# Kernel optimization log

Measured on AMD Instinct MI355X. Metric: run time of the kernel, lower is better.

## Reference

```python
import jax, jax.numpy as jnp
import numpy as np

N = 100000
IN_C, HID, OUT_D, NUM_CLASSES = 256, 64, 64, 6
E = 1600000


def setup_inputs() -> dict:
    key = jax.random.key(0)
    ks = jax.random.split(key, 12)
    glorot = lambda k, fi, fo: jax.random.normal(k, (fi, fo), jnp.float32) * np.sqrt(2.0 / (fi + fo))
    return {
        "x": jax.random.normal(ks[0], (N, IN_C), jnp.float32),
        "edge_index": jax.random.randint(ks[1], (2, E), 0, N, jnp.int64),
        "W1": glorot(ks[2], IN_C, HID), "b1": jnp.zeros((HID,), jnp.float32),
        "W2": glorot(ks[3], HID, HID), "b2": jnp.zeros((HID,), jnp.float32),
        "Wp": glorot(ks[4], HID, OUT_D), "bp": jnp.zeros((OUT_D,), jnp.float32),
        "Wc": glorot(ks[5], OUT_D, NUM_CLASSES), "bc": jnp.zeros((NUM_CLASSES,), jnp.float32),
    }


def _gcn_norm(edge_index, n):
    # add self-loops, symmetric normalization D^{-1/2}(A+I)D^{-1/2} (PyG gcn_norm)
    loop = jnp.arange(n, dtype=edge_index.dtype)
    src = jnp.concatenate([edge_index[0], loop])
    dst = jnp.concatenate([edge_index[1], loop])
    deg = jax.ops.segment_sum(jnp.ones_like(dst, jnp.float32), dst, num_segments=n)
    dinv = jnp.where(deg > 0, jax.lax.rsqrt(deg), 0.0)
    norm = dinv[src] * dinv[dst]  # [E+N]
    return src, dst, norm


def _gcn_conv(x, W, b, src, dst, norm, n):
    h = x @ W  # dense GEMM first (PyG order)
    msg = h[src] * norm[:, None]  # gather + scale over edges
    out = jax.ops.segment_sum(msg, dst, num_segments=n)  # scatter-add aggregate
    return out + b


def reference(x, edge_index, W1, b1, W2, b2, Wp, bp, Wc, bc):
    n = x.shape[0]
    src, dst, norm = _gcn_norm(edge_index, n)
    h = jax.nn.relu(_gcn_conv(x, W1, b1, src, dst, norm, n))
    # dropout is inactive in eval mode (training=False)
    h = jax.nn.relu(_gcn_conv(h, W2, b2, src, dst, norm, n))
    z = jax.nn.relu(h @ Wp + bp)
    logits = z @ Wc + bc
    return (logits, z)
```

## Files before the change

kernel.cpp:

```cpp
#include <hip/hip_runtime.h>

#define N_NODES 100000
#define IN_CH   256
#define HID_D   64
#define NCLS    6
#define NE      1600000
#define WB      48
#define OVF_CAP 4096
#define NPART   8
#define PSZ     (N_NODES / NPART)

typedef unsigned short u16;
typedef unsigned int   u32;
typedef __attribute__((ext_vector_type(8))) short bf16x8;
typedef __attribute__((ext_vector_type(4))) float f32x4;
typedef __attribute__((ext_vector_type(2))) int   i32x2;

#define OFF_CNT   0u
#define OFF_OVFC  400000u
#define OFF_OVF   400128u
#define OFF_COL   433152u
#define OFF_WT    19633152u
#define OFF_G     19684480u
#define OFF_H     32484480u
#define WT_W1 0
#define WT_W2 16384
#define WT_WP 20480
#define WT_WC 24576
#define WT_TOT 25600
#define Z_OFF 600000u

__device__ __forceinline__ u16 f2bf(float f) {
    u32 u = __float_as_uint(f);
    return (u16)((u + 0x7fffu + ((u >> 16) & 1u)) >> 16);
}
__device__ __forceinline__ float bf2f(u16 h) {
    return __uint_as_float(((u32)h) << 16);
}

__global__ __launch_bounds__(256) void k_wprep(const float* __restrict__ W1,
                                               const float* __restrict__ W2,
                                               const float* __restrict__ Wp,
                                               const float* __restrict__ Wc,
                                               u16* __restrict__ wt) {
    int m = blockIdx.x * 256 + threadIdx.x;
    if (m >= WT_TOT) return;
    float v;
    if (m >= WT_WC) {
        int i = m - WT_WC;
        int j = i & 7, l = (i >> 3) & 63, kk = i >> 9;
        int k = kk * 32 + (l >> 4) * 8 + j;
        int c = l & 15;
        v = (c < NCLS) ? Wc[k * NCLS + c] : 0.f;
    } else {
        const float* src; int i;
        if      (m < WT_W2) { src = W1; i = m - WT_W1; }
        else if (m < WT_WP) { src = W2; i = m - WT_W2; }
        else                { src = Wp; i = m - WT_WP; }
        int j = i & 7, l = (i >> 3) & 63, t = (i >> 9) & 3, kk = i >> 11;
        int k = kk * 32 + (l >> 4) * 8 + j;
        int c = t * 16 + (l & 15);
        v = src[k * 64 + c];
    }
    wt[m] = f2bf(v);
}

__global__ __launch_bounds__(256) void k_fill(const int* __restrict__ ei,
                                              int* __restrict__ cnt,
                                              int* __restrict__ col,
                                              int* __restrict__ ovfc,
                                              int* __restrict__ ovf) {
    const int part = blockIdx.x & (NPART - 1);
    const int lo = part * PSZ;
    const int hi = lo + PSZ;
    const int e0 = (blockIdx.x >> 3) * 512 + threadIdx.x * 2;
    i32x2 s2 = __builtin_nontemporal_load((const i32x2*)(ei + e0));
    i32x2 d2 = __builtin_nontemporal_load((const i32x2*)(ei + NE + e0));
#pragma unroll
    for (int j = 0; j < 2; ++j) {
        int s = s2[j];
        int d = d2[j];
        if (d < lo || d >= hi) continue;
        if ((u32)s >= (u32)N_NODES) continue;
        int p = atomicAdd(&cnt[d], 1);
        if (p < WB) {
            col[(size_t)d * WB + p] = s;
        } else {
            int k = atomicAdd(ovfc, 1);
            if (k < OVF_CAP) { ovf[2 * k] = s; ovf[2 * k + 1] = d; }
        }
    }
}

template <int KDIM, bool ABF16>
__global__ __launch_bounds__(256) void k_gemm(const void* __restrict__ A,
                                              const u16* __restrict__ wt,
                                              const int* __restrict__ cnt,
                                              u16* __restrict__ G) {
    constexpr int KK = KDIM / 32;
    __shared__ __align__(16) u16 sB[KK * 2048];

    for (int idx = threadIdx.x * 8; idx < KK * 2048; idx += 2048)
        *(bf16x8*)&sB[idx] = *(const bf16x8*)&wt[idx];
    __syncthreads();

    const int lane = threadIdx.x & 63;
    const int wv   = threadIdx.x >> 6;
    const int row0 = blockIdx.x * 64 + wv * 16;
    const int g4   = lane >> 4;
    const int r16  = lane & 15;

    int arow = row0 + r16;
    int arow_c = arow < N_NODES ? arow : 0;

    f32x4 acc[4] = {{0,0,0,0},{0,0,0,0},{0,0,0,0},{0,0,0,0}};

#pragma unroll
    for (int kk = 0; kk < KK; ++kk) {
        bf16x8 a;
        if (ABF16) {
            a = *(const bf16x8*)((const u16*)A + (size_t)arow_c * KDIM + kk * 32 + g4 * 8);
        } else {
            const float* ap = (const float*)A + (size_t)arow_c * KDIM + kk * 32 + g4 * 8;
            float4 f0 = *(const float4*)ap;
            float4 f1 = *(const float4*)(ap + 4);
            a[0] = (short)f2bf(f0.x); a[1] = (short)f2bf(f0.y);
            a[2] = (short)f2bf(f0.z); a[3] = (short)f2bf(f0.w);
            a[4] = (short)f2bf(f1.x); a[5] = (short)f2bf(f1.y);
            a[6] = (short)f2bf(f1.z); a[7] = (short)f2bf(f1.w);
        }
#pragma unroll
        for (int t = 0; t < 4; ++t) {
            bf16x8 b = *(const bf16x8*)&sB[((kk * 4 + t) * 64 + lane) * 8];
            acc[t] = __builtin_amdgcn_mfma_f32_16x16x32_bf16(a, b, acc[t], 0, 0, 0);
        }
    }

#pragma unroll
    for (int r = 0; r < 4; ++r) {
        int row = row0 + g4 * 4 + r;
        if (row < N_NODES) {
            float dinv = rsqrtf((float)(cnt[row] + 1));
#pragma unroll
            for (int t = 0; t < 4; ++t)
                G[(size_t)row * 64 + t * 16 + r16] = f2bf(acc[t][r] * dinv);
        }
    }
}

__global__ __launch_bounds__(256) void k_agg(const u16* __restrict__ G,
                                             const int* __restrict__ col,
                                             const int* __restrict__ cnt,
                                             const int* __restrict__ ovfc,
                                             const int* __restrict__ ovf,
                                             const float* __restrict__ bias,
                                             u16* __restrict__ Hout) {
    int node = blockIdx.x * 4 + (threadIdx.x >> 6);
    int lane = threadIdx.x & 63;

    int deg = cnt[node];
    int m = min(deg, WB);
    int mycol = (lane < WB) ? col[(size_t)node * WB + lane] : 0;

    float acc = bf2f(G[(size_t)node * 64 + lane]);

    int e = 0;
    for (; e + 4 <= m; e += 4) {
        int c0 = __shfl(mycol, e + 0), c1 = __shfl(mycol, e + 1);
        int c2 = __shfl(mycol, e + 2), c3 = __shfl(mycol, e + 3);
        float v0 = bf2f(G[(size_t)c0 * 64 + lane]);
        float v1 = bf2f(G[(size_t)c1 * 64 + lane]);
        float v2 = bf2f(G[(size_t)c2 * 64 + lane]);
        float v3 = bf2f(G[(size_t)c3 * 64 + lane]);
        acc += v0; acc += v1; acc += v2; acc += v3;
    }
    for (; e < m; ++e) {
        int c = __shfl(mycol, e);
        acc += bf2f(G[(size_t)c * 64 + lane]);
    }

    int no = *ovfc;
    if (no > 0) {
        no = min(no, OVF_CAP);
        for (int j = 0; j < no; ++j)
            if (ovf[2 * j + 1] == node)
                acc += bf2f(G[(size_t)ovf[2 * j] * 64 + lane]);
    }

    float dinv = rsqrtf((float)(deg + 1));
    float v = fmaxf(acc * dinv + bias[lane], 0.f);
    Hout[(size_t)node * 64 + lane] = f2bf(v);
}

__global__ __launch_bounds__(256) void k_mlp(const u16* __restrict__ H,
                                             const u16* __restrict__ wt,
                                             const float* __restrict__ bp,
                                             const float* __restrict__ bc,
                                             float* __restrict__ out) {
    __shared__ __align__(16) u16 sP[2 * 2048];
    __shared__ __align__(16) u16 sC[1024];
    __shared__ __align__(16) u16 zt[4][16][72];

    for (int idx = threadIdx.x * 8; idx < 4096; idx += 2048)
        *(bf16x8*)&sP[idx] = *(const bf16x8*)&wt[WT_WP + idx];
    {
        int idx = threadIdx.x * 8;
        if (idx < 1024)
            *(bf16x8*)&sC[idx] = *(const bf16x8*)&wt[WT_WC + idx];
    }
    __syncthreads();

    const int lane = threadIdx.x & 63;
    const int wv   = threadIdx.x >> 6;
    const int row0 = blockIdx.x * 64 + wv * 16;
    const int g4   = lane >> 4;
    const int r16  = lane & 15;

    int arow = row0 + r16;
    int arow_c = arow < N_NODES ? arow : (N_NODES - 1);

    f32x4 zac[4] = {{0,0,0,0},{0,0,0,0},{0,0,0,0},{0,0,0,0}};
#pragma unroll
    for (int kk = 0; kk < 2; ++kk) {
        bf16x8 a = *(const bf16x8*)((const u16*)H + (size_t)arow_c * 64 + kk * 32 + g4 * 8);
#pragma unroll
        for (int t = 0; t < 4; ++t) {
            bf16x8 b = *(const bf16x8*)&sP[((kk * 4 + t) * 64 + lane) * 8];
            zac[t] = __builtin_amdgcn_mfma_f32_16x16x32_bf16(a, b, zac[t], 0, 0, 0);
        }
    }

#pragma unroll
    for (int r = 0; r < 4; ++r) {
        int row = row0 + g4 * 4 + r;
#pragma unroll
        for (int t = 0; t < 4; ++t) {
            float v = zac[t][r] + bp[t * 16 + r16];
            v = fmaxf(v, 0.f);
            zt[wv][g4 * 4 + r][t * 16 + r16] = f2bf(v);
            if (row < N_NODES)
                out[(size_t)Z_OFF + (size_t)row * 64 + t * 16 + r16] = v;
        }
    }
    __syncthreads();

    f32x4 lac = {0, 0, 0, 0};
#pragma unroll
    for (int kk = 0; kk < 2; ++kk) {
        bf16x8 a = *(const bf16x8*)&zt[wv][r16][kk * 32 + g4 * 8];
        bf16x8 b = *(const bf16x8*)&sC[(kk * 64 + lane) * 8];
        lac = __builtin_amdgcn_mfma_f32_16x16x32_bf16(a, b, lac, 0, 0, 0);
    }
#pragma unroll
    for (int r = 0; r < 4; ++r) {
        int row = row0 + g4 * 4 + r;
        if (row < N_NODES && r16 < NCLS)
            out[(size_t)row * NCLS + r16] = lac[r] + bc[r16];
    }
}

extern "C" void kernel_launch(void* const* d_in, const int* in_sizes, int n_in,
                              void* d_out, int out_size, void* d_ws, size_t ws_size,
                              hipStream_t stream) {
    const float* x  = (const float*)d_in[0];
    const int*   ei = (const int*)d_in[1];
    const float* W1 = (const float*)d_in[2];
    const float* b1 = (const float*)d_in[3];
    const float* W2 = (const float*)d_in[4];
    const float* b2 = (const float*)d_in[5];
    const float* Wp = (const float*)d_in[6];
    const float* bp = (const float*)d_in[7];
    const float* Wc = (const float*)d_in[8];
    const float* bc = (const float*)d_in[9];
    float* out = (float*)d_out;

    char* ws   = (char*)d_ws;
    int*  cnt  = (int*)(ws + OFF_CNT);
    int*  ovfc = (int*)(ws + OFF_OVFC);
    int*  ovf  = (int*)(ws + OFF_OVF);
    int*  col  = (int*)(ws + OFF_COL);
    u16*  wt   = (u16*)(ws + OFF_WT);
    u16*  g    = (u16*)(ws + OFF_G);
    u16*  h    = (u16*)(ws + OFF_H);

    const int GB = (N_NODES + 63) / 64;

    (void)hipMemsetAsync(ws, 0, OFF_OVF, stream);
    k_wprep<<<WT_TOT / 256, 256, 0, stream>>>(W1, W2, Wp, Wc, wt);
    k_fill<<<(NE / 512) * NPART, 256, 0, stream>>>(ei, cnt, col, ovfc, ovf);
    k_gemm<IN_CH, false><<<GB, 256, 0, stream>>>(x, wt + WT_W1, cnt, g);
    k_agg<<<N_NODES / 4, 256, 0, stream>>>(g, col, cnt, ovfc, ovf, b1, h);
    k_gemm<HID_D, true><<<GB, 256, 0, stream>>>(h, wt + WT_W2, cnt, g);
    k_agg<<<N_NODES / 4, 256, 0, stream>>>(g, col, cnt, ovfc, ovf, b2, h);
    k_mlp<<<GB, 256, 0, stream>>>(h, wt, bp, bc, out);
}
```

Baseline: 222.7 us.

## Replace partitioned edge fill with two-pass bucketed partition then per-partition insert

The old fill kernel read every edge once per destination partition (eight passes over edge_index) and inserted only the matching ones. The new version reads edges once, uses wave ballots to stage them in shared memory by destination partition, and writes per-block partition queues to a scratch buffer that reuses the G region. A second kernel then drains each partition's queues with partition-affine blocks, so atomics stay localized. This adds an extra intermediate write and read of edges plus shared-memory staging, with overflow falling back to direct inserts.

Result: slower. 230.2 us (+3.4%).

```diff
diff --git a/kernel.cpp b/kernel.cpp
--- a/kernel.cpp
+++ b/kernel.cpp
@@ -9,9 +9,13 @@
 #define OVF_CAP 4096
 #define NPART   8
 #define PSZ     (N_NODES / NPART)
+#define NBLK    3125
+#define SCAP    56
+#define BCAP    128
 
 typedef unsigned short u16;
 typedef unsigned int   u32;
+typedef unsigned long long u64;
 typedef __attribute__((ext_vector_type(8))) short bf16x8;
 typedef __attribute__((ext_vector_type(4))) float f32x4;
 typedef __attribute__((ext_vector_type(2))) int   i32x2;
@@ -23,6 +27,8 @@
 #define OFF_WT    19633152u
 #define OFF_G     19684480u
 #define OFF_H     32484480u
+#define OFF_QBUF  OFF_G
+#define OFF_QN    45284480u
 #define WT_W1 0
 #define WT_W2 16384
 #define WT_WP 20480
@@ -36,6 +42,20 @@
 }
 __device__ __forceinline__ float bf2f(u16 h) {
     return __uint_as_float(((u32)h) << 16);
+}
+
+__device__ __forceinline__ void bucket_insert(int s, int d,
+                                              int* __restrict__ cnt,
+                                              int* __restrict__ col,
+                                              int* __restrict__ ovfc,
+                                              int* __restrict__ ovf) {
+    int p = atomicAdd(&cnt[d], 1);
+    if (p < WB) {
+        col[(size_t)d * WB + p] = s;
+    } else {
+        int k = atomicAdd(ovfc, 1);
+        if (k < OVF_CAP) { ovf[2 * k] = s; ovf[2 * k + 1] = d; }
+    }
 }
 
 __global__ __launch_bounds__(256) void k_wprep(const float* __restrict__ W1,
@@ -65,29 +85,81 @@
     wt[m] = f2bf(v);
 }
 
-__global__ __launch_bounds__(256) void k_fill(const int* __restrict__ ei,
-                                              int* __restrict__ cnt,
-                                              int* __restrict__ col,
-                                              int* __restrict__ ovfc,
-                                              int* __restrict__ ovf) {
-    const int part = blockIdx.x & (NPART - 1);
-    const int lo = part * PSZ;
-    const int hi = lo + PSZ;
-    const int e0 = (blockIdx.x >> 3) * 512 + threadIdx.x * 2;
+__global__ __launch_bounds__(256) void k_part2(const int* __restrict__ ei,
+                                               int2* __restrict__ qbuf,
+                                               int* __restrict__ qn,
+                                               int* __restrict__ cnt,
+                                               int* __restrict__ col,
+                                               int* __restrict__ ovfc,
+                                               int* __restrict__ ovf) {
+    __shared__ int2 stage[4][NPART][SCAP];
+    __shared__ int  wn[4][NPART];
+    const int tid = threadIdx.x, lane = tid & 63, w = tid >> 6;
+    const int b = blockIdx.x;
+    const int e0 = b * 512 + tid * 2;
     i32x2 s2 = __builtin_nontemporal_load((const i32x2*)(ei + e0));
     i32x2 d2 = __builtin_nontemporal_load((const i32x2*)(ei + NE + e0));
+    const u64 lmask = (lane == 63) ? ~0ull >> 1 : (1ull << lane) - 1ull;
+
+    int bq[NPART] = {0, 0, 0, 0, 0, 0, 0, 0};
 #pragma unroll
     for (int j = 0; j < 2; ++j) {
         int s = s2[j];
         int d = d2[j];
-        if (d < lo || d >= hi) continue;
-        if ((u32)s >= (u32)N_NODES) continue;
-        int p = atomicAdd(&cnt[d], 1);
-        if (p < WB) {
-            col[(size_t)d * WB + p] = s;
-        } else {
-            int k = atomicAdd(ovfc, 1);
-            if (k < OVF_CAP) { ovf[2 * k] = s; ovf[2 * k + 1] = d; }
+        int p = (u32)d < (u32)N_NODES ? d / PSZ : NPART;
+#pragma unroll
+        for (int q = 0; q < NPART; ++q) {
+            u64 m = __ballot(p == q);
+            if (p == q) {
+                int idx = bq[q] + __popcll(m & lmask);
+                if (idx < SCAP) stage[w][q][idx] = make_int2(s, d);
+                else bucket_insert(s, d, cnt, col, ovfc, ovf);
+            }
+            bq[q] += __popcll(m);
+        }
+    }
+    if (lane < NPART) wn[w][lane] = min(bq[lane], SCAP);
+    __syncthreads();
+
+#pragma unroll
+    for (int qq = 0; qq < 2; ++qq) {
+        int q = w * 2 + qq;
+        int n0 = wn[0][q], n1 = wn[1][q], n2 = wn[2][q], n3 = wn[3][q];
+        int tot = n0 + n1 + n2 + n3;
+        int2* dst = qbuf + ((size_t)q * NBLK + b) * BCAP;
+        for (int i = lane; i < tot; i += 64) {
+            int wi, idx;
+            if      (i < n0)           { wi = 0; idx = i; }
+            else if (i < n0 + n1)      { wi = 1; idx = i - n0; }
+            else if (i < n0 + n1 + n2) { wi = 2; idx = i - n0 - n1; }
+            else                       { wi = 3; idx = i - n0 - n1 - n2; }
+            int2 e = stage[wi][q][idx];
+            if (i < BCAP) dst[i] = e;
+            else bucket_insert(e.x, e.y, cnt, col, ovfc, ovf);
+        }
+        if (lane == 0) qn[q * NBLK + b] = min(tot, BCAP);
+    }
+}
+
+__global__ __launch_bounds__(256) void k_fill3(const int2* __restrict__ qbuf,
+                                               const int* __restrict__ qn,
+                                               int* __restrict__ cnt,
+                                               int* __restrict__ col,
+                                               int* __restrict__ ovfc,
+                                               int* __restrict__ ovf) {
+    const int part = blockIdx.x & (NPART - 1);
+    const int lane = threadIdx.x & 63;
+    const int w    = threadIdx.x >> 6;
+    const int gstep = (gridDim.x >> 3) * 4;
+    for (int b0 = (blockIdx.x >> 3) * 4; b0 < NBLK; b0 += gstep) {
+        int b = b0 + w;
+        if (b < NBLK) {
+            int n = qn[part * NBLK + b];
+            const int2* q = qbuf + ((size_t)part * NBLK + b) * BCAP;
+            for (int i = lane; i < n; i += 64) {
+                i32x2 e = __builtin_nontemporal_load((const i32x2*)q + i);
+                bucket_insert(e[0], e[1], cnt, col, ovfc, ovf);
+            }
         }
     }
 }
@@ -280,6 +352,8 @@
     int*  ovf  = (int*)(ws + OFF_OVF);
     int*  col  = (int*)(ws + OFF_COL);
     u16*  wt   = (u16*)(ws + OFF_WT);
+    int2* qbuf = (int2*)(ws + OFF_QBUF);
+    int*  qn   = (int*)(ws + OFF_QN);
     u16*  g    = (u16*)(ws + OFF_G);
     u16*  h    = (u16*)(ws + OFF_H);
 
@@ -287,7 +361,8 @@
 
     (void)hipMemsetAsync(ws, 0, OFF_OVF, stream);
     k_wprep<<<WT_TOT / 256, 256, 0, stream>>>(W1, W2, Wp, Wc, wt);
-    k_fill<<<(NE / 512) * NPART, 256, 0, stream>>>(ei, cnt, col, ovfc, ovf);
+    k_part2<<<NBLK, 256, 0, stream>>>(ei, qbuf, qn, cnt, col, ovfc, ovf);
+    k_fill3<<<128 * NPART, 256, 0, stream>>>(qbuf, qn, cnt, col, ovfc, ovf);
     k_gemm<IN_CH, false><<<GB, 256, 0, stream>>>(x, wt + WT_W1, cnt, g);
     k_agg<<<N_NODES / 4, 256, 0, stream>>>(g, col, cnt, ovfc, ovf, b1, h);
     k_gemm<HID_D, true><<<GB, 256, 0, stream>>>(h, wt + WT_W2, cnt, g);
```

## Fuse edge fill with first GEMM and move degree normalization into aggregation

Applied to the files above, without the earlier changes.

The edge-bucketing fill and the first feature GEMM now run as one launch with disjoint block ranges, so the atomic-heavy fill can overlap the bandwidth-bound read of x. Because degrees are not final while the GEMM runs, the GEMMs no longer pre-scale by the source dinv. Instead the aggregation kernel gathers each neighbour's count and applies rsqrt per edge, and applies the destination dinv to the self term and to the final sum. The memset is replaced by zeroing the counters inside the weight-prep kernel. The cost of this is one extra small gather and multiply per edge in both aggregation passes.

Result: slower. 233.8 us (+4.9%).

```diff
diff --git a/kernel.cpp b/kernel.cpp
--- a/kernel.cpp
+++ b/kernel.cpp
@@ -9,6 +9,8 @@
 #define OVF_CAP 4096
 #define NPART   8
 #define PSZ     (N_NODES / NPART)
+#define FILLB   ((NE / 512) * NPART)
+#define GEMMB   1563
 
 typedef unsigned short u16;
 typedef unsigned int   u32;
@@ -42,8 +44,10 @@
                                                const float* __restrict__ W2,
                                                const float* __restrict__ Wp,
                                                const float* __restrict__ Wc,
-                                               u16* __restrict__ wt) {
+                                               u16* __restrict__ wt,
+                                               int* __restrict__ cntz) {
     int m = blockIdx.x * 256 + threadIdx.x;
+    for (int i = m; i <= N_NODES; i += 25600) cntz[i] = 0;
     if (m >= WT_TOT) return;
     float v;
     if (m >= WT_WC) {
@@ -65,42 +69,88 @@
     wt[m] = f2bf(v);
 }
 
-__global__ __launch_bounds__(256) void k_fill(const int* __restrict__ ei,
-                                              int* __restrict__ cnt,
-                                              int* __restrict__ col,
-                                              int* __restrict__ ovfc,
-                                              int* __restrict__ ovf) {
-    const int part = blockIdx.x & (NPART - 1);
-    const int lo = part * PSZ;
-    const int hi = lo + PSZ;
-    const int e0 = (blockIdx.x >> 3) * 512 + threadIdx.x * 2;
-    i32x2 s2 = __builtin_nontemporal_load((const i32x2*)(ei + e0));
-    i32x2 d2 = __builtin_nontemporal_load((const i32x2*)(ei + NE + e0));
-#pragma unroll
-    for (int j = 0; j < 2; ++j) {
-        int s = s2[j];
-        int d = d2[j];
-        if (d < lo || d >= hi) continue;
-        if ((u32)s >= (u32)N_NODES) continue;
-        int p = atomicAdd(&cnt[d], 1);
-        if (p < WB) {
-            col[(size_t)d * WB + p] = s;
-        } else {
-            int k = atomicAdd(ovfc, 1);
-            if (k < OVF_CAP) { ovf[2 * k] = s; ovf[2 * k + 1] = d; }
-        }
-    }
-}
-
-template <int KDIM, bool ABF16>
-__global__ __launch_bounds__(256) void k_gemm(const void* __restrict__ A,
-                                              const u16* __restrict__ wt,
-                                              const int* __restrict__ cnt,
-                                              u16* __restrict__ G) {
-    constexpr int KK = KDIM / 32;
-    __shared__ __align__(16) u16 sB[KK * 2048];
-
-    for (int idx = threadIdx.x * 8; idx < KK * 2048; idx += 2048)
+__global__ __launch_bounds__(256) void k_fillgemm(const int* __restrict__ ei,
+                                                  int* __restrict__ cnt,
+                                                  int* __restrict__ col,
+                                                  int* __restrict__ ovfc,
+                                                  int* __restrict__ ovf,
+                                                  const float* __restrict__ x,
+                                                  const u16* __restrict__ wt,
+                                                  u16* __restrict__ G) {
+    __shared__ __align__(16) u16 sB[8 * 2048];
+
+    if (blockIdx.x < FILLB) {
+        const int part = blockIdx.x & (NPART - 1);
+        const int lo = part * PSZ;
+        const int hi = lo + PSZ;
+        const int e0 = (blockIdx.x >> 3) * 512 + threadIdx.x * 2;
+        i32x2 s2 = __builtin_nontemporal_load((const i32x2*)(ei + e0));
+        i32x2 d2 = __builtin_nontemporal_load((const i32x2*)(ei + NE + e0));
+#pragma unroll
+        for (int j = 0; j < 2; ++j) {
+            int s = s2[j];
+            int d = d2[j];
+            if (d < lo || d >= hi) continue;
+            if ((u32)s >= (u32)N_NODES) continue;
+            int p = atomicAdd(&cnt[d], 1);
+            if (p < WB) {
+                col[(size_t)d * WB + p] = s;
+            } else {
+                int k = atomicAdd(ovfc, 1);
+                if (k < OVF_CAP) { ovf[2 * k] = s; ovf[2 * k + 1] = d; }
+            }
+        }
+        return;
+    }
+
+    const int gb = blockIdx.x - FILLB;
+    for (int idx = threadIdx.x * 8; idx < 16384; idx += 2048)
+        *(bf16x8*)&sB[idx] = *(const bf16x8*)&wt[idx];
+    __syncthreads();
+
+    const int lane = threadIdx.x & 63;
+    const int wv   = threadIdx.x >> 6;
+    const int row0 = gb * 64 + wv * 16;
+    const int g4   = lane >> 4;
+    const int r16  = lane & 15;
+
+    int arow = row0 + r16;
+    int arow_c = arow < N_NODES ? arow : 0;
+
+    f32x4 acc[4] = {{0,0,0,0},{0,0,0,0},{0,0,0,0},{0,0,0,0}};
+
+#pragma unroll
+    for (int kk = 0; kk < 8; ++kk) {
+        const float* ap = x + (size_t)arow_c * IN_CH + kk * 32 + g4 * 8;
+        float4 f0 = *(const float4*)ap;
+        float4 f1 = *(const float4*)(ap + 4);
+        bf16x8 a;
+        a[0] = (short)f2bf(f0.x); a[1] = (short)f2bf(f0.y);
+        a[2] = (short)f2bf(f0.z); a[3] = (short)f2bf(f0.w);
+        a[4] = (short)f2bf(f1.x); a[5] = (short)f2bf(f1.y);
+        a[6] = (short)f2bf(f1.z); a[7] = (short)f2bf(f1.w);
+#pragma unroll
+        for (int t = 0; t < 4; ++t) {
+            bf16x8 b = *(const bf16x8*)&sB[((kk * 4 + t) * 64 + lane) * 8];
+            acc[t] = __builtin_amdgcn_mfma_f32_16x16x32_bf16(a, b, acc[t], 0, 0, 0);
+        }
+    }
+
+#pragma unroll
+    for (int r = 0; r < 4; ++r) {
+        int row = row0 + g4 * 4 + r;
+        if (row < N_NODES)
+#pragma unroll
+            for (int t = 0; t < 4; ++t)
+                G[(size_t)row * 64 + t * 16 + r16] = f2bf(acc[t][r]);
+    }
+}
+
+__global__ __launch_bounds__(256) void k_gemm2(const u16* __restrict__ A,
+                                               const u16* __restrict__ wt,
+                                               u16* __restrict__ G) {
+    __shared__ __align__(16) u16 sB[2 * 2048];
+    for (int idx = threadIdx.x * 8; idx < 4096; idx += 2048)
         *(bf16x8*)&sB[idx] = *(const bf16x8*)&wt[idx];
     __syncthreads();
 
@@ -114,37 +164,22 @@
     int arow_c = arow < N_NODES ? arow : 0;
 
     f32x4 acc[4] = {{0,0,0,0},{0,0,0,0},{0,0,0,0},{0,0,0,0}};
-
-#pragma unroll
-    for (int kk = 0; kk < KK; ++kk) {
-        bf16x8 a;
-        if (ABF16) {
-            a = *(const bf16x8*)((const u16*)A + (size_t)arow_c * KDIM + kk * 32 + g4 * 8);
-        } else {
-            const float* ap = (const float*)A + (size_t)arow_c * KDIM + kk * 32 + g4 * 8;
-            float4 f0 = *(const float4*)ap;
-            float4 f1 = *(const float4*)(ap + 4);
-            a[0] = (short)f2bf(f0.x); a[1] = (short)f2bf(f0.y);
-            a[2] = (short)f2bf(f0.z); a[3] = (short)f2bf(f0.w);
-            a[4] = (short)f2bf(f1.x); a[5] = (short)f2bf(f1.y);
-            a[6] = (short)f2bf(f1.z); a[7] = (short)f2bf(f1.w);
-        }
+#pragma unroll
+    for (int kk = 0; kk < 2; ++kk) {
+        bf16x8 a = *(const bf16x8*)(A + (size_t)arow_c * 64 + kk * 32 + g4 * 8);
 #pragma unroll
         for (int t = 0; t < 4; ++t) {
             bf16x8 b = *(const bf16x8*)&sB[((kk * 4 + t) * 64 + lane) * 8];
             acc[t] = __builtin_amdgcn_mfma_f32_16x16x32_bf16(a, b, acc[t], 0, 0, 0);
         }
     }
-
 #pragma unroll
     for (int r = 0; r < 4; ++r) {
         int row = row0 + g4 * 4 + r;
-        if (row < N_NODES) {
-            float dinv = rsqrtf((float)(cnt[row] + 1));
+        if (row < N_NODES)
 #pragma unroll
             for (int t = 0; t < 4; ++t)
-                G[(size_t)row * 64 + t * 16 + r16] = f2bf(acc[t][r] * dinv);
-        }
+                G[(size_t)row * 64 + t * 16 + r16] = f2bf(acc[t][r]);
     }
 }
 
@@ -160,35 +195,41 @@
 
     int deg = cnt[node];
     int m = min(deg, WB);
-    int mycol = (lane < WB) ? col[(size_t)node * WB + lane] : 0;
-
-    float acc = bf2f(G[(size_t)node * 64 + lane]);
+    float dinv_i = rsqrtf((float)(deg + 1));
+
+    int mycol = (lane < m) ? col[(size_t)node * WB + lane] : 0;
+    float mydinv = rsqrtf((float)(cnt[mycol] + 1));
+
+    float acc = dinv_i * bf2f(G[(size_t)node * 64 + lane]);
 
     int e = 0;
     for (; e + 4 <= m; e += 4) {
         int c0 = __shfl(mycol, e + 0), c1 = __shfl(mycol, e + 1);
         int c2 = __shfl(mycol, e + 2), c3 = __shfl(mycol, e + 3);
-        float v0 = bf2f(G[(size_t)c0 * 64 + lane]);
-        float v1 = bf2f(G[(size_t)c1 * 64 + lane]);
-        float v2 = bf2f(G[(size_t)c2 * 64 + lane]);
-        float v3 = bf2f(G[(size_t)c3 * 64 + lane]);
-        acc += v0; acc += v1; acc += v2; acc += v3;
+        float w0 = __shfl(mydinv, e + 0), w1 = __shfl(mydinv, e + 1);
+        float w2 = __shfl(mydinv, e + 2), w3 = __shfl(mydinv, e + 3);
+        acc += w0 * bf2f(G[(size_t)c0 * 64 + lane]);
+        acc += w1 * bf2f(G[(size_t)c1 * 64 + lane]);
+        acc += w2 * bf2f(G[(size_t)c2 * 64 + lane]);
+        acc += w3 * bf2f(G[(size_t)c3 * 64 + lane]);
     }
     for (; e < m; ++e) {
         int c = __shfl(mycol, e);
-        acc += bf2f(G[(size_t)c * 64 + lane]);
+        float w = __shfl(mydinv, e);
+        acc += w * bf2f(G[(size_t)c * 64 + lane]);
     }
 
     int no = *ovfc;
     if (no > 0) {
         no = min(no, OVF_CAP);
         for (int j = 0; j < no; ++j)
-            if (ovf[2 * j + 1] == node)
-                acc += bf2f(G[(size_t)ovf[2 * j] * 64 + lane]);
-    }
-
-    float dinv = rsqrtf((float)(deg + 1));
-    float v = fmaxf(acc * dinv + bias[lane], 0.f);
+            if (ovf[2 * j + 1] == node) {
+                int s = ovf[2 * j];
+                acc += rsqrtf((float)(cnt[s] + 1)) * bf2f(G[(size_t)s * 64 + lane]);
+            }
+    }
+
+    float v = fmaxf(dinv_i * acc + bias[lane], 0.f);
     Hout[(size_t)node * 64 + lane] = f2bf(v);
 }
 
@@ -283,14 +324,10 @@
     u16*  g    = (u16*)(ws + OFF_G);
     u16*  h    = (u16*)(ws + OFF_H);
 
-    const int GB = (N_NODES + 63) / 64;
-
-    (void)hipMemsetAsync(ws, 0, OFF_OVF, stream);
-    k_wprep<<<WT_TOT / 256, 256, 0, stream>>>(W1, W2, Wp, Wc, wt);
-    k_fill<<<(NE / 512) * NPART, 256, 0, stream>>>(ei, cnt, col, ovfc, ovf);
-    k_gemm<IN_CH, false><<<GB, 256, 0, stream>>>(x, wt + WT_W1, cnt, g);
+    k_wprep<<<100, 256, 0, stream>>>(W1, W2, Wp, Wc, wt, cnt);
+    k_fillgemm<<<FILLB + GEMMB, 256, 0, stream>>>(ei, cnt, col, ovfc, ovf, x, wt, g);
     k_agg<<<N_NODES / 4, 256, 0, stream>>>(g, col, cnt, ovfc, ovf, b1, h);
-    k_gemm<HID_D, true><<<GB, 256, 0, stream>>>(h, wt + WT_W2, cnt, g);
+    k_gemm2<<<GEMMB, 256, 0, stream>>>(h, wt + WT_W2, g);
     k_agg<<<N_NODES / 4, 256, 0, stream>>>(g, col, cnt, ovfc, ovf, b2, h);
-    k_mlp<<<GB, 256, 0, stream>>>(h, wt, bp, bc, out);
-}
+    k_mlp<<<GEMMB, 256, 0, stream>>>(h, wt, bp, bc, out);
+}
```
